# Performance work log

Measured on AMD Instinct MI355X. Metric: run time of the kernel, lower is better.

## Reference

```python
import jax, jax.numpy as jnp
import numpy as np

N_NODES = 100000
N_EDGES = 1600000
N_GRAPHS = 1024
D_IN = 128
D_HID = 128
D_OUT = 2


def setup_inputs() -> dict:
    key = jax.random.key(0)
    ks = jax.random.split(key, 12)
    x = jax.random.normal(ks[0], (N_NODES, D_IN), dtype=jnp.float32)
    edge_index = jax.random.randint(ks[1], (2, N_EDGES), 0, N_NODES, dtype=jnp.int32)
    batch = jnp.sort(jax.random.randint(ks[2], (N_NODES,), 0, N_GRAPHS, dtype=jnp.int32))
    def lin(k, fan_in, fan_out):
        bound = 1.0 / np.sqrt(fan_in)
        kw, kb = jax.random.split(k)
        W = jax.random.uniform(kw, (fan_in, fan_out), minval=-bound, maxval=bound, dtype=jnp.float32)
        b = jax.random.uniform(kb, (fan_out,), minval=-bound, maxval=bound, dtype=jnp.float32)
        return W, b
    W1, b1 = lin(ks[3], D_IN, D_HID)
    W2, b2 = lin(ks[4], D_HID, D_HID)
    fc1_w, fc1_b = lin(ks[5], D_HID, D_HID)
    fc2_w, fc2_b = lin(ks[6], D_HID, D_OUT)
    return {"x": x, "edge_index": edge_index, "batch": batch,
            "W1": W1, "b1": b1, "W2": W2, "b2": b2,
            "fc1_w": fc1_w, "fc1_b": fc1_b, "fc2_w": fc2_w, "fc2_b": fc2_b}


def gcn_conv(x, W, b, src, dst, deg_inv_sqrt, n_nodes):
    # GCNConv: out = D^-1/2 (A + I) D^-1/2 (x W) + b, using edge list with self-loops
    h = x @ W  # [N, d_out]
    norm = deg_inv_sqrt[src] * deg_inv_sqrt[dst]  # [E+N]
    msg = h[src] * norm[:, None]  # gather + scale
    out = jnp.zeros((n_nodes, h.shape[1]), dtype=h.dtype).at[dst].add(msg)
    return out + b


def reference(x, edge_index, batch, W1, b1, W2, b2, fc1_w, fc1_b, fc2_w, fc2_b):
    n = x.shape[0]
    loops = jnp.arange(n, dtype=edge_index.dtype)
    src = jnp.concatenate([edge_index[0], loops])  # add self-loops (PyG default)
    dst = jnp.concatenate([edge_index[1], loops])
    deg = jnp.zeros((n,), dtype=x.dtype).at[dst].add(1.0)
    deg_inv_sqrt = jax.lax.rsqrt(deg)  # deg >= 1 due to self-loops

    h = jax.nn.relu(gcn_conv(x, W1, b1, src, dst, deg_inv_sqrt, n))
    # dropout p=0.5 is identity in eval mode
    h = jax.nn.relu(gcn_conv(h, W2, b2, src, dst, deg_inv_sqrt, n))

    # global_mean_pool over batch assignment
    sums = jax.ops.segment_sum(h, batch, num_segments=N_GRAPHS)
    cnts = jax.ops.segment_sum(jnp.ones((n,), dtype=h.dtype), batch, num_segments=N_GRAPHS)
    pooled = sums / jnp.maximum(cnts, 1.0)[:, None]  # [G, d]

    g = jax.nn.relu(pooled @ fc1_w + fc1_b)
    logits = g @ fc2_w + fc2_b
    return jax.nn.log_softmax(logits, axis=1)
```

## Files before the change

kernel.cpp:

```cpp
#include <hip/hip_runtime.h>
#include <hip/hip_fp16.h>
#include <math.h>


#define D_FEAT 128
#define BSHIFT 9
#define BNODES 512
#define CHUNK 4096
#define CAP 10240
#define CAPB 16384

using half8   = __attribute__((ext_vector_type(8))) _Float16;
using half4   = __attribute__((ext_vector_type(4))) _Float16;
using floatx4 = __attribute__((ext_vector_type(4))) float;
using floatx2 = __attribute__((ext_vector_type(2))) float;

__global__ void __launch_bounds__(256) binA_kernel(const int* __restrict__ edges,
                                                   int* __restrict__ gcur,
                                                   int* __restrict__ binned, int E, int nb) {
    __shared__ int h[256];
    __shared__ int cur[256];
    __shared__ int base[256];
    int t = threadIdx.x;
    int c0 = blockIdx.x * CHUNK;
    int sv[CHUNK / 256], bv[CHUNK / 256];
    int i0 = c0 + t * (CHUNK / 256);
    if (i0 + (CHUNK / 256) <= E) {
#pragma unroll
        for (int k = 0; k < CHUNK / 256; k += 4) {
            int4 s4 = *(const int4*)&edges[i0 + k];
            int4 d4 = *(const int4*)&edges[E + i0 + k];
            bv[k + 0] = d4.x >> BSHIFT; sv[k + 0] = ((d4.x & (BNODES - 1)) << 17) | s4.x;
            bv[k + 1] = d4.y >> BSHIFT; sv[k + 1] = ((d4.y & (BNODES - 1)) << 17) | s4.y;
            bv[k + 2] = d4.z >> BSHIFT; sv[k + 2] = ((d4.z & (BNODES - 1)) << 17) | s4.z;
            bv[k + 3] = d4.w >> BSHIFT; sv[k + 3] = ((d4.w & (BNODES - 1)) << 17) | s4.w;
        }
    } else {
#pragma unroll
        for (int k = 0; k < CHUNK / 256; ++k) {
            int i = i0 + k;
            if (i < E) {
                int s = edges[i], d = edges[E + i];
                bv[k] = d >> BSHIFT;
                sv[k] = ((d & (BNODES - 1)) << 17) | s;
            } else bv[k] = -1;
        }
    }
    h[t] = 0;
    __syncthreads();
#pragma unroll
    for (int k = 0; k < CHUNK / 256; ++k)
        if (bv[k] >= 0) atomicAdd(&h[bv[k]], 1);
    __syncthreads();
    if (t < nb && h[t] > 0) base[t] = atomicAdd(&gcur[t], h[t]);
    cur[t] = 0;
    __syncthreads();
#pragma unroll
    for (int k = 0; k < CHUNK / 256; ++k)
        if (bv[k] >= 0) {
            int b = bv[k];
            int r = atomicAdd(&cur[b], 1);
            int pos = base[b] + r;
            if (pos < CAPB) binned[b * CAPB + pos] = sv[k];
        }
}

__global__ void bucket_scan_kernel(const int* __restrict__ gcur, int* __restrict__ bucketBase,
                                   int nb, int E) {
    __shared__ int sdata[256];
    int t = threadIdx.x;
    int v = (t < nb) ? gcur[t] : 0;
    sdata[t] = v;
    __syncthreads();
    for (int d = 1; d < 256; d <<= 1) {
        int u = (t >= d) ? sdata[t - d] : 0;
        __syncthreads();
        sdata[t] += u;
        __syncthreads();
    }
    if (t < nb) bucketBase[t] = sdata[t] - v;
    if (t == 0) bucketBase[nb] = E;
}

__global__ void __launch_bounds__(256) binB_kernel(const int* __restrict__ binned,
                                                   const int* __restrict__ bucketBase,
                                                   const int* __restrict__ gcur,
                                                   float* __restrict__ dis,
                                                   int* __restrict__ rowptr,
                                                   int* __restrict__ csr_src,
                                                   int N, int E, int nb) {
    __shared__ int hist[BNODES];
    __shared__ int cursorA[BNODES];
    __shared__ int sdata[256];
    __shared__ int vals[CAP];
    int t = threadIdx.x;
    int b = blockIdx.x;
    int node0 = b << BSHIFT;
    int e0 = bucketBase[b];
    int cnt = gcur[b];
    const int* bin = binned + (size_t)b * CAPB;
    hist[t] = 0; hist[t + 256] = 0;
    __syncthreads();
    for (int i = t; i < cnt; i += 256) {
        int v = bin[i];
        if (i < CAP) vals[i] = v;
        atomicAdd(&hist[v >> 17], 1);
    }
    __syncthreads();
    int a0 = hist[2 * t], a1 = hist[2 * t + 1];
    int pair = a0 + a1;
    sdata[t] = pair;
    __syncthreads();
    for (int d = 1; d < 256; d <<= 1) {
        int u = (t >= d) ? sdata[t - d] : 0;
        __syncthreads();
        sdata[t] += u;
        __syncthreads();
    }
    int excl = sdata[t] - pair;
    int p0 = e0 + excl, p1 = e0 + excl + a0;
    cursorA[2 * t] = p0;
    cursorA[2 * t + 1] = p1;
    int n0 = node0 + 2 * t, n1 = node0 + 2 * t + 1;
    if (n0 < N) { rowptr[n0] = p0; dis[n0] = rsqrtf((float)a0 + 1.0f); }
    if (n1 < N) { rowptr[n1] = p1; dis[n1] = rsqrtf((float)a1 + 1.0f); }
    if (b == nb - 1 && t == 0) rowptr[N] = E;
    __syncthreads();
    for (int i = t; i < cnt; i += 256) {
        int v = (i < CAP) ? vals[i] : bin[i];
        int p = atomicAdd(&cursorA[v >> 17], 1);
        csr_src[p] = v & 0x1FFFF;
    }
}

__global__ void wprep_kernel(const float* __restrict__ W1, const float* __restrict__ W2,
                             _Float16* __restrict__ Wt1, _Float16* __restrict__ Wt2) {
    int i = blockIdx.x * blockDim.x + threadIdx.x;
    int n = i >> 7, k = i & 127;
    Wt1[i] = (_Float16)W1[k * 128 + n];
    Wt2[i] = (_Float16)W2[k * 128 + n];
}

template <bool HALF_IN>
__global__ void __launch_bounds__(512) gemm_mfma_kernel(const void* __restrict__ Xv,
                                                        const _Float16* __restrict__ WtG,
                                                        unsigned char* __restrict__ Y8, int N) {
    __shared__ _Float16 wt[128][136];
    __shared__ _Float16 xs[128][136];
    int t = threadIdx.x;
    int row0 = blockIdx.x * 128;

#pragma unroll
    for (int i = 0; i < 4; ++i) {
        int c = t + i * 512;
        int r = c >> 4, c8 = (c & 15) * 8;
        *(half8*)&wt[r][c8] = *(const half8*)&WtG[r * 128 + c8];
    }
    {
        int r = t >> 2, cb = (t & 3) * 32;
        int grow = row0 + r;
        if (HALF_IN) {
            const _Float16* Xp = (const _Float16*)Xv;
#pragma unroll
            for (int i = 0; i < 4; ++i) {
                half8 v = {};
                if (grow < N) v = *(const half8*)&Xp[(size_t)grow * 128 + cb + i * 8];
                *(half8*)&xs[r][cb + i * 8] = v;
            }
        } else {
            const float* Xp = (const float*)Xv;
#pragma unroll
            for (int i = 0; i < 8; ++i) {
                float4 v = make_float4(0.f, 0.f, 0.f, 0.f);
                if (grow < N) v = *(const float4*)&Xp[(size_t)grow * 128 + cb + i * 4];
                half4 h = {(_Float16)v.x, (_Float16)v.y, (_Float16)v.z, (_Float16)v.w};
                *(half4*)&xs[r][cb + i * 4] = h;
            }
        }
    }
    __syncthreads();

    int wave = t >> 6, lane = t & 63;
    int m = lane & 15, quad = lane >> 4;
    int wrow = wave * 16;

    half8 a[4];
#pragma unroll
    for (int k = 0; k < 4; ++k) a[k] = *(const half8*)&xs[wrow + m][k * 32 + quad * 8];

    floatx4 acc[8];
#pragma unroll
    for (int nt = 0; nt < 8; ++nt) acc[nt] = (floatx4){0.f, 0.f, 0.f, 0.f};
#pragma unroll
    for (int nt = 0; nt < 8; ++nt) {
#pragma unroll
        for (int k = 0; k < 4; ++k) {
            half8 bfr = *(const half8*)&wt[nt * 16 + m][k * 32 + quad * 8];
            acc[nt] = __builtin_amdgcn_mfma_f32_16x16x32_f16(a[k], bfr, acc[nt], 0, 0, 0);
        }
    }
#pragma unroll
    for (int nt = 0; nt < 8; ++nt) {
#pragma unroll
        for (int r = 0; r < 4; ++r) {
            int row = row0 + wrow + quad * 4 + r;
            if (row < N) {
                float v = acc[nt][r];
                unsigned char q =
                    (unsigned char)(__builtin_amdgcn_cvt_pk_fp8_f32(v, v, 0, false) & 0xff);
                Y8[(size_t)row * 128 + nt * 16 + m] = q;
            }
        }
    }
}

__global__ void __launch_bounds__(256) agg_kernel(const unsigned char* __restrict__ H8,
                                                  const int* __restrict__ rowptr,
                                                  const int* __restrict__ csr_src,
                                                  const float* __restrict__ dis,
                                                  const float* __restrict__ bias,
                                                  _Float16* __restrict__ out, int N) {
    int v = (blockIdx.x * blockDim.x + threadIdx.x) >> 6;
    int lane = threadIdx.x & 63;
    if (v >= N) return;
    int half = lane >> 5, sl = lane & 31;
    int r0 = rowptr[v], r1 = rowptr[v + 1];
    float dv = dis[v];

    float a0, a1, a2, a3;
    {
        float wself = 0.5f * dv * dv;
        unsigned int u = *(const unsigned int*)(H8 + (size_t)v * 128 + sl * 4);
        floatx2 lo = __builtin_amdgcn_cvt_pk_f32_fp8(u, false);
        floatx2 hi = __builtin_amdgcn_cvt_pk_f32_fp8(u, true);
        a0 = wself * lo[0]; a1 = wself * lo[1];
        a2 = wself * hi[0]; a3 = wself * hi[1];
    }
    int e = r0 + half;
    for (; e + 6 < r1; e += 8) {
        int s0 = csr_src[e], s1 = csr_src[e + 2], s2 = csr_src[e + 4], s3 = csr_src[e + 6];
        float w0 = dis[s0] * dv, w1 = dis[s1] * dv, w2 = dis[s2] * dv, w3 = dis[s3] * dv;
        unsigned int u0 = *(const unsigned int*)(H8 + (size_t)s0 * 128 + sl * 4);
        unsigned int u1 = *(const unsigned int*)(H8 + (size_t)s1 * 128 + sl * 4);
        unsigned int u2 = *(const unsigned int*)(H8 + (size_t)s2 * 128 + sl * 4);
        unsigned int u3 = *(const unsigned int*)(H8 + (size_t)s3 * 128 + sl * 4);
        floatx2 l0 = __builtin_amdgcn_cvt_pk_f32_fp8(u0, false);
        floatx2 h0 = __builtin_amdgcn_cvt_pk_f32_fp8(u0, true);
        floatx2 l1 = __builtin_amdgcn_cvt_pk_f32_fp8(u1, false);
        floatx2 h1 = __builtin_amdgcn_cvt_pk_f32_fp8(u1, true);
        floatx2 l2 = __builtin_amdgcn_cvt_pk_f32_fp8(u2, false);
        floatx2 h2 = __builtin_amdgcn_cvt_pk_f32_fp8(u2, true);
        floatx2 l3 = __builtin_amdgcn_cvt_pk_f32_fp8(u3, false);
        floatx2 h3 = __builtin_amdgcn_cvt_pk_f32_fp8(u3, true);
        a0 += w0 * l0[0] + w1 * l1[0] + w2 * l2[0] + w3 * l3[0];
        a1 += w0 * l0[1] + w1 * l1[1] + w2 * l2[1] + w3 * l3[1];
        a2 += w0 * h0[0] + w1 * h1[0] + w2 * h2[0] + w3 * h3[0];
        a3 += w0 * h0[1] + w1 * h1[1] + w2 * h2[1] + w3 * h3[1];
    }
    for (; e < r1; e += 2) {
        int s0 = csr_src[e];
        float w0 = dis[s0] * dv;
        unsigned int u0 = *(const unsigned int*)(H8 + (size_t)s0 * 128 + sl * 4);
        floatx2 l0 = __builtin_amdgcn_cvt_pk_f32_fp8(u0, false);
        floatx2 h0 = __builtin_amdgcn_cvt_pk_f32_fp8(u0, true);
        a0 += w0 * l0[0]; a1 += w0 * l0[1];
        a2 += w0 * h0[0]; a3 += w0 * h0[1];
    }
    a0 += __shfl_xor(a0, 32, 64);
    a1 += __shfl_xor(a1, 32, 64);
    a2 += __shfl_xor(a2, 32, 64);
    a3 += __shfl_xor(a3, 32, 64);
    if (half == 0) {
        float4 b = *(const float4*)&bias[sl * 4];
        half4 o = {(_Float16)fmaxf(a0 + b.x, 0.f), (_Float16)fmaxf(a1 + b.y, 0.f),
                   (_Float16)fmaxf(a2 + b.z, 0.f), (_Float16)fmaxf(a3 + b.w, 0.f)};
        *(half4*)&out[(size_t)v * 128 + sl * 4] = o;
    }
}

__device__ __forceinline__ int lower_bound_i(const int* a, int n, int key) {
    int lo = 0, hi = n;
    while (lo < hi) {
        int mid = (lo + hi) >> 1;
        if (a[mid] < key) lo = mid + 1;
        else hi = mid;
    }
    return lo;
}

__global__ void __launch_bounds__(512) pool_kernel(const _Float16* __restrict__ H,
                                                   const int* __restrict__ batch,
                                                   float* __restrict__ pooled, int N) {
    __shared__ int range[2];
    __shared__ float part[4][128];
    int g = blockIdx.x;
    int t = threadIdx.x;
    int j = t & 127, rg = t >> 7;
    if (t < 2) range[t] = lower_bound_i(batch, N, g + t);
    __syncthreads();
    int lo = range[0], hi = range[1];
    float s = 0.f;
    for (int v = lo + rg; v < hi; v += 4) s += (float)H[(size_t)v * 128 + j];
    part[rg][j] = s;
    __syncthreads();
    if (rg == 0) {
        float tot = part[0][j] + part[1][j] + part[2][j] + part[3][j];
        pooled[g * 128 + j] = tot / fmaxf((float)(hi - lo), 1.0f);
    }
}

__global__ void head_kernel(const float* __restrict__ pooled, const float* __restrict__ fc1w,
                            const float* __restrict__ fc1b, const float* __restrict__ fc2w,
                            const float* __restrict__ fc2b, float* __restrict__ out) {
    __shared__ float p[128];
    __shared__ float r0[128], r1[128];
    int g = blockIdx.x;
    int j = threadIdx.x;
    p[j] = pooled[g * 128 + j];
    __syncthreads();
    float acc = fc1b[j];
#pragma unroll 8
    for (int k = 0; k < 128; ++k) acc = fmaf(p[k], fc1w[k * 128 + j], acc);
    float gv = fmaxf(acc, 0.f);
    r0[j] = gv * fc2w[j * 2 + 0];
    r1[j] = gv * fc2w[j * 2 + 1];
    __syncthreads();
    for (int s = 64; s > 0; s >>= 1) {
        if (j < s) {
            r0[j] += r0[j + s];
            r1[j] += r1[j + s];
        }
        __syncthreads();
    }
    if (j == 0) {
        float l0 = r0[0] + fc2b[0];
        float l1 = r1[0] + fc2b[1];
        float m = fmaxf(l0, l1);
        float lse = m + logf(expf(l0 - m) + expf(l1 - m));
        out[g * 2 + 0] = l0 - lse;
        out[g * 2 + 1] = l1 - lse;
    }
}

extern "C" void kernel_launch(void* const* d_in, const int* in_sizes, int n_in,
                              void* d_out, int out_size, void* d_ws, size_t ws_size,
                              hipStream_t stream) {
    const float* x    = (const float*)d_in[0];
    const int* edges  = (const int*)d_in[1];
    const int* batch  = (const int*)d_in[2];
    const float* W1   = (const float*)d_in[3];
    const float* b1   = (const float*)d_in[4];
    const float* W2   = (const float*)d_in[5];
    const float* b2   = (const float*)d_in[6];
    const float* fc1w = (const float*)d_in[7];
    const float* fc1b = (const float*)d_in[8];
    const float* fc2w = (const float*)d_in[9];
    const float* fc2b = (const float*)d_in[10];
    float* out = (float*)d_out;

    int N = in_sizes[2];
    int E = in_sizes[1] / 2;
    int G = out_size / 2;
    int nb = (N + BNODES - 1) / BNODES;
    int nA = (E + CHUNK - 1) / CHUNK;

    char* ws = (char*)d_ws;
    size_t off = 0;
    auto alloc = [&](size_t bytes) -> char* {
        char* ptr = ws + off;
        off += (bytes + 255) & ~(size_t)255;
        return ptr;
    };
    int* gcur          = (int*)alloc((size_t)nb * 4);
    int* bucketBase    = (int*)alloc((size_t)(nb + 1) * 4);
    int* binned        = (int*)alloc((size_t)nb * CAPB * 4);
    int* rowptr        = (int*)alloc((size_t)(N + 1) * 4);
    float* dis         = (float*)alloc((size_t)N * 4);
    int* csr_src       = (int*)alloc((size_t)E * 4);
    _Float16* Wt1      = (_Float16*)alloc(128 * 128 * 2);
    _Float16* Wt2      = (_Float16*)alloc(128 * 128 * 2);
    unsigned char* buf8 = (unsigned char*)alloc((size_t)N * D_FEAT);
    _Float16* bufH     = (_Float16*)alloc((size_t)N * D_FEAT * 2);
    float* pooled      = (float*)alloc((size_t)G * D_FEAT * 4);

    hipMemsetAsync(gcur, 0, (size_t)nb * 4, stream);

    binA_kernel<<<nA, 256, 0, stream>>>(edges, gcur, binned, E, nb);
    bucket_scan_kernel<<<1, 256, 0, stream>>>(gcur, bucketBase, nb, E);
    binB_kernel<<<nb, 256, 0, stream>>>(binned, bucketBase, gcur, dis, rowptr, csr_src, N, E, nb);
    wprep_kernel<<<64, 256, 0, stream>>>(W1, W2, Wt1, Wt2);

    const int tb = 256;
    int gAgg = (N * 64 + tb - 1) / tb;
    int gGemm = (N + 127) / 128;
    gemm_mfma_kernel<false><<<gGemm, 512, 0, stream>>>((const void*)x, Wt1, buf8, N);
    agg_kernel<<<gAgg, tb, 0, stream>>>(buf8, rowptr, csr_src, dis, b1, bufH, N);
    gemm_mfma_kernel<true><<<gGemm, 512, 0, stream>>>((const void*)bufH, Wt2, buf8, N);
    agg_kernel<<<gAgg, tb, 0, stream>>>(buf8, rowptr, csr_src, dis, b2, bufH, N);
    pool_kernel<<<G, 512, 0, stream>>>(bufH, batch, pooled, N);
    head_kernel<<<G, 128, 0, stream>>>(pooled, fc1w, fc1b, fc2w, fc2b, out);
}
```

Before: 312.1 us.

## Precompute edge norms into int2 CSR, split binB, load GEMM A directly

The CSR build is split into two kernels. The second writes (src, norm) pairs, so the aggregation no longer does a dependent dis[src] gather per edge. The aggregation loop is unrolled to 8 edges per half-wave to keep more gathers in flight. The GEMM now loads A fragments straight from global memory into registers, uses 64-row blocks with 256 threads, and drops the X shared-memory staging. In exchange the CSR doubles to 8 bytes per edge, there is an extra launch, and gcursor is round-tripped through global memory.

```diff
diff --git a/kernel.cpp b/kernel.cpp
--- a/kernel.cpp
+++ b/kernel.cpp
@@ -7,7 +7,6 @@
 #define BSHIFT 9
 #define BNODES 512
 #define CHUNK 4096
-#define CAP 10240
 #define CAPB 16384
 
 using half8   = __attribute__((ext_vector_type(8))) _Float16;
@@ -82,17 +81,15 @@
     if (t == 0) bucketBase[nb] = E;
 }
 
-__global__ void __launch_bounds__(256) binB_kernel(const int* __restrict__ binned,
-                                                   const int* __restrict__ bucketBase,
-                                                   const int* __restrict__ gcur,
-                                                   float* __restrict__ dis,
-                                                   int* __restrict__ rowptr,
-                                                   int* __restrict__ csr_src,
-                                                   int N, int E, int nb) {
+__global__ void __launch_bounds__(256) binB1_kernel(const int* __restrict__ binned,
+                                                    const int* __restrict__ bucketBase,
+                                                    const int* __restrict__ gcur,
+                                                    float* __restrict__ dis,
+                                                    int* __restrict__ rowptr,
+                                                    int* __restrict__ gcursor,
+                                                    int N, int E, int nb) {
     __shared__ int hist[BNODES];
-    __shared__ int cursorA[BNODES];
     __shared__ int sdata[256];
-    __shared__ int vals[CAP];
     int t = threadIdx.x;
     int b = blockIdx.x;
     int node0 = b << BSHIFT;
@@ -101,11 +98,7 @@
     const int* bin = binned + (size_t)b * CAPB;
     hist[t] = 0; hist[t + 256] = 0;
     __syncthreads();
-    for (int i = t; i < cnt; i += 256) {
-        int v = bin[i];
-        if (i < CAP) vals[i] = v;
-        atomicAdd(&hist[v >> 17], 1);
-    }
+    for (int i = t; i < cnt; i += 256) atomicAdd(&hist[bin[i] >> 17], 1);
     __syncthreads();
     int a0 = hist[2 * t], a1 = hist[2 * t + 1];
     int pair = a0 + a1;
@@ -119,17 +112,41 @@
     }
     int excl = sdata[t] - pair;
     int p0 = e0 + excl, p1 = e0 + excl + a0;
-    cursorA[2 * t] = p0;
-    cursorA[2 * t + 1] = p1;
+    gcursor[(b << BSHIFT) + 2 * t] = p0;
+    gcursor[(b << BSHIFT) + 2 * t + 1] = p1;
     int n0 = node0 + 2 * t, n1 = node0 + 2 * t + 1;
     if (n0 < N) { rowptr[n0] = p0; dis[n0] = rsqrtf((float)a0 + 1.0f); }
     if (n1 < N) { rowptr[n1] = p1; dis[n1] = rsqrtf((float)a1 + 1.0f); }
     if (b == nb - 1 && t == 0) rowptr[N] = E;
+}
+
+__global__ void __launch_bounds__(256) binB2_kernel(const int* __restrict__ binned,
+                                                    const int* __restrict__ gcur,
+                                                    const int* __restrict__ gcursor,
+                                                    const float* __restrict__ dis,
+                                                    int2* __restrict__ csr,
+                                                    int N, int nb) {
+    __shared__ int cur[BNODES];
+    __shared__ float dloc[BNODES];
+    int t = threadIdx.x;
+    int b = blockIdx.x;
+    int node0 = b << BSHIFT;
+    int cnt = gcur[b];
+    const int* bin = binned + (size_t)b * CAPB;
+#pragma unroll
+    for (int i = 0; i < 2; ++i) {
+        int idx = t + i * 256;
+        cur[idx] = gcursor[(b << BSHIFT) + idx];
+        int n = node0 + idx;
+        dloc[idx] = (n < N) ? dis[n] : 0.f;
+    }
     __syncthreads();
     for (int i = t; i < cnt; i += 256) {
-        int v = (i < CAP) ? vals[i] : bin[i];
-        int p = atomicAdd(&cursorA[v >> 17], 1);
-        csr_src[p] = v & 0x1FFFF;
+        int v = bin[i];
+        int dstl = v >> 17, s = v & 0x1FFFF;
+        int p = atomicAdd(&cur[dstl], 1);
+        float nrm = dis[s] * dloc[dstl];
+        csr[p] = make_int2(s, __float_as_int(nrm));
     }
 }
 
@@ -142,51 +159,46 @@
 }
 
 template <bool HALF_IN>
-__global__ void __launch_bounds__(512) gemm_mfma_kernel(const void* __restrict__ Xv,
+__global__ void __launch_bounds__(256) gemm_mfma_kernel(const void* __restrict__ Xv,
                                                         const _Float16* __restrict__ WtG,
                                                         unsigned char* __restrict__ Y8, int N) {
     __shared__ _Float16 wt[128][136];
-    __shared__ _Float16 xs[128][136];
-    int t = threadIdx.x;
-    int row0 = blockIdx.x * 128;
-
-#pragma unroll
-    for (int i = 0; i < 4; ++i) {
-        int c = t + i * 512;
+    int t = threadIdx.x;
+    int row0 = blockIdx.x * 64;
+
+#pragma unroll
+    for (int i = 0; i < 8; ++i) {
+        int c = t + i * 256;
         int r = c >> 4, c8 = (c & 15) * 8;
         *(half8*)&wt[r][c8] = *(const half8*)&WtG[r * 128 + c8];
     }
-    {
-        int r = t >> 2, cb = (t & 3) * 32;
-        int grow = row0 + r;
+
+    int wave = t >> 6, lane = t & 63;
+    int m = lane & 15, quad = lane >> 4;
+    int grow = row0 + wave * 16 + m;
+
+    half8 a[4];
+    if (grow < N) {
         if (HALF_IN) {
             const _Float16* Xp = (const _Float16*)Xv;
 #pragma unroll
-            for (int i = 0; i < 4; ++i) {
-                half8 v = {};
-                if (grow < N) v = *(const half8*)&Xp[(size_t)grow * 128 + cb + i * 8];
-                *(half8*)&xs[r][cb + i * 8] = v;
-            }
+            for (int k = 0; k < 4; ++k)
+                a[k] = *(const half8*)&Xp[(size_t)grow * 128 + k * 32 + quad * 8];
         } else {
             const float* Xp = (const float*)Xv;
 #pragma unroll
-            for (int i = 0; i < 8; ++i) {
-                float4 v = make_float4(0.f, 0.f, 0.f, 0.f);
-                if (grow < N) v = *(const float4*)&Xp[(size_t)grow * 128 + cb + i * 4];
-                half4 h = {(_Float16)v.x, (_Float16)v.y, (_Float16)v.z, (_Float16)v.w};
-                *(half4*)&xs[r][cb + i * 4] = h;
+            for (int k = 0; k < 4; ++k) {
+                float4 v0 = *(const float4*)&Xp[(size_t)grow * 128 + k * 32 + quad * 8];
+                float4 v1 = *(const float4*)&Xp[(size_t)grow * 128 + k * 32 + quad * 8 + 4];
+                a[k] = (half8){(_Float16)v0.x, (_Float16)v0.y, (_Float16)v0.z, (_Float16)v0.w,
+                               (_Float16)v1.x, (_Float16)v1.y, (_Float16)v1.z, (_Float16)v1.w};
             }
         }
-    }
-    __syncthreads();
-
-    int wave = t >> 6, lane = t & 63;
-    int m = lane & 15, quad = lane >> 4;
-    int wrow = wave * 16;
-
-    half8 a[4];
-#pragma unroll
-    for (int k = 0; k < 4; ++k) a[k] = *(const half8*)&xs[wrow + m][k * 32 + quad * 8];
+    } else {
+#pragma unroll
+        for (int k = 0; k < 4; ++k) a[k] = (half8){};
+    }
+    __syncthreads();
 
     floatx4 acc[8];
 #pragma unroll
@@ -203,7 +215,7 @@
     for (int nt = 0; nt < 8; ++nt) {
 #pragma unroll
         for (int r = 0; r < 4; ++r) {
-            int row = row0 + wrow + quad * 4 + r;
+            int row = row0 + wave * 16 + quad * 4 + r;
             if (row < N) {
                 float v = acc[nt][r];
                 unsigned char q =
@@ -216,7 +228,7 @@
 
 __global__ void __launch_bounds__(256) agg_kernel(const unsigned char* __restrict__ H8,
                                                   const int* __restrict__ rowptr,
-                                                  const int* __restrict__ csr_src,
+                                                  const int2* __restrict__ csr,
                                                   const float* __restrict__ dis,
                                                   const float* __restrict__ bias,
                                                   _Float16* __restrict__ out, int N) {
@@ -237,35 +249,38 @@
         a2 = wself * hi[0]; a3 = wself * hi[1];
     }
     int e = r0 + half;
-    for (; e + 6 < r1; e += 8) {
-        int s0 = csr_src[e], s1 = csr_src[e + 2], s2 = csr_src[e + 4], s3 = csr_src[e + 6];
-        float w0 = dis[s0] * dv, w1 = dis[s1] * dv, w2 = dis[s2] * dv, w3 = dis[s3] * dv;
-        unsigned int u0 = *(const unsigned int*)(H8 + (size_t)s0 * 128 + sl * 4);
-        unsigned int u1 = *(const unsigned int*)(H8 + (size_t)s1 * 128 + sl * 4);
-        unsigned int u2 = *(const unsigned int*)(H8 + (size_t)s2 * 128 + sl * 4);
-        unsigned int u3 = *(const unsigned int*)(H8 + (size_t)s3 * 128 + sl * 4);
-        floatx2 l0 = __builtin_amdgcn_cvt_pk_f32_fp8(u0, false);
-        floatx2 h0 = __builtin_amdgcn_cvt_pk_f32_fp8(u0, true);
-        floatx2 l1 = __builtin_amdgcn_cvt_pk_f32_fp8(u1, false);
-        floatx2 h1 = __builtin_amdgcn_cvt_pk_f32_fp8(u1, true);
-        floatx2 l2 = __builtin_amdgcn_cvt_pk_f32_fp8(u2, false);
-        floatx2 h2 = __builtin_amdgcn_cvt_pk_f32_fp8(u2, true);
-        floatx2 l3 = __builtin_amdgcn_cvt_pk_f32_fp8(u3, false);
-        floatx2 h3 = __builtin_amdgcn_cvt_pk_f32_fp8(u3, true);
-        a0 += w0 * l0[0] + w1 * l1[0] + w2 * l2[0] + w3 * l3[0];
-        a1 += w0 * l0[1] + w1 * l1[1] + w2 * l2[1] + w3 * l3[1];
-        a2 += w0 * h0[0] + w1 * h1[0] + w2 * h2[0] + w3 * h3[0];
-        a3 += w0 * h0[1] + w1 * h1[1] + w2 * h2[1] + w3 * h3[1];
+    for (; e + 14 < r1; e += 16) {
+        int2 c0 = csr[e],      c1 = csr[e + 2],  c2 = csr[e + 4],  c3 = csr[e + 6];
+        int2 c4 = csr[e + 8],  c5 = csr[e + 10], c6 = csr[e + 12], c7 = csr[e + 14];
+        unsigned int u0 = *(const unsigned int*)(H8 + (size_t)c0.x * 128 + sl * 4);
+        unsigned int u1 = *(const unsigned int*)(H8 + (size_t)c1.x * 128 + sl * 4);
+        unsigned int u2 = *(const unsigned int*)(H8 + (size_t)c2.x * 128 + sl * 4);
+        unsigned int u3 = *(const unsigned int*)(H8 + (size_t)c3.x * 128 + sl * 4);
+        unsigned int u4 = *(const unsigned int*)(H8 + (size_t)c4.x * 128 + sl * 4);
+        unsigned int u5 = *(const unsigned int*)(H8 + (size_t)c5.x * 128 + sl * 4);
+        unsigned int u6 = *(const unsigned int*)(H8 + (size_t)c6.x * 128 + sl * 4);
+        unsigned int u7 = *(const unsigned int*)(H8 + (size_t)c7.x * 128 + sl * 4);
+        float w0 = __int_as_float(c0.y), w1 = __int_as_float(c1.y);
+        float w2 = __int_as_float(c2.y), w3 = __int_as_float(c3.y);
+        float w4 = __int_as_float(c4.y), w5 = __int_as_float(c5.y);
+        float w6 = __int_as_float(c6.y), w7 = __int_as_float(c7.y);
+#define ACC(uu, ww)                                                     \
+        {                                                               \
+            floatx2 lo = __builtin_amdgcn_cvt_pk_f32_fp8(uu, false);    \
+            floatx2 hi = __builtin_amdgcn_cvt_pk_f32_fp8(uu, true);     \
+            a0 += (ww) * lo[0]; a1 += (ww) * lo[1];                     \
+            a2 += (ww) * hi[0]; a3 += (ww) * hi[1];                     \
+        }
+        ACC(u0, w0) ACC(u1, w1) ACC(u2, w2) ACC(u3, w3)
+        ACC(u4, w4) ACC(u5, w5) ACC(u6, w6) ACC(u7, w7)
     }
     for (; e < r1; e += 2) {
-        int s0 = csr_src[e];
-        float w0 = dis[s0] * dv;
-        unsigned int u0 = *(const unsigned int*)(H8 + (size_t)s0 * 128 + sl * 4);
-        floatx2 l0 = __builtin_amdgcn_cvt_pk_f32_fp8(u0, false);
-        floatx2 h0 = __builtin_amdgcn_cvt_pk_f32_fp8(u0, true);
-        a0 += w0 * l0[0]; a1 += w0 * l0[1];
-        a2 += w0 * h0[0]; a3 += w0 * h0[1];
-    }
+        int2 c0 = csr[e];
+        float w0 = __int_as_float(c0.y);
+        unsigned int u0 = *(const unsigned int*)(H8 + (size_t)c0.x * 128 + sl * 4);
+        ACC(u0, w0)
+    }
+#undef ACC
     a0 += __shfl_xor(a0, 32, 64);
     a1 += __shfl_xor(a1, 32, 64);
     a2 += __shfl_xor(a2, 32, 64);
@@ -376,7 +391,8 @@
     int* binned        = (int*)alloc((size_t)nb * CAPB * 4);
     int* rowptr        = (int*)alloc((size_t)(N + 1) * 4);
     float* dis         = (float*)alloc((size_t)N * 4);
-    int* csr_src       = (int*)alloc((size_t)E * 4);
+    int* gcursor       = (int*)alloc((size_t)nb * BNODES * 4);
+    int2* csr          = (int2*)alloc((size_t)E * 8);
     _Float16* Wt1      = (_Float16*)alloc(128 * 128 * 2);
     _Float16* Wt2      = (_Float16*)alloc(128 * 128 * 2);
     unsigned char* buf8 = (unsigned char*)alloc((size_t)N * D_FEAT);
@@ -387,16 +403,17 @@
 
     binA_kernel<<<nA, 256, 0, stream>>>(edges, gcur, binned, E, nb);
     bucket_scan_kernel<<<1, 256, 0, stream>>>(gcur, bucketBase, nb, E);
-    binB_kernel<<<nb, 256, 0, stream>>>(binned, bucketBase, gcur, dis, rowptr, csr_src, N, E, nb);
+    binB1_kernel<<<nb, 256, 0, stream>>>(binned, bucketBase, gcur, dis, rowptr, gcursor, N, E, nb);
+    binB2_kernel<<<nb, 256, 0, stream>>>(binned, gcur, gcursor, dis, csr, N, nb);
     wprep_kernel<<<64, 256, 0, stream>>>(W1, W2, Wt1, Wt2);
 
     const int tb = 256;
     int gAgg = (N * 64 + tb - 1) / tb;
-    int gGemm = (N + 127) / 128;
-    gemm_mfma_kernel<false><<<gGemm, 512, 0, stream>>>((const void*)x, Wt1, buf8, N);
-    agg_kernel<<<gAgg, tb, 0, stream>>>(buf8, rowptr, csr_src, dis, b1, bufH, N);
-    gemm_mfma_kernel<true><<<gGemm, 512, 0, stream>>>((const void*)bufH, Wt2, buf8, N);
-    agg_kernel<<<gAgg, tb, 0, stream>>>(buf8, rowptr, csr_src, dis, b2, bufH, N);
+    int gGemm = (N + 63) / 64;
+    gemm_mfma_kernel<false><<<gGemm, 256, 0, stream>>>((const void*)x, Wt1, buf8, N);
+    agg_kernel<<<gAgg, tb, 0, stream>>>(buf8, rowptr, csr, dis, b1, bufH, N);
+    gemm_mfma_kernel<true><<<gGemm, 256, 0, stream>>>((const void*)bufH, Wt2, buf8, N);
+    agg_kernel<<<gAgg, tb, 0, stream>>>(buf8, rowptr, csr, dis, b2, bufH, N);
     pool_kernel<<<G, 512, 0, stream>>>(bufH, batch, pooled, N);
     head_kernel<<<G, 128, 0, stream>>>(pooled, fc1w, fc1b, fc2w, fc2b, out);
 }
```

After: 357.2 us. +14.4%, slower.
